# Kernel optimization log

Measured on AMD Instinct MI355X. Metric: run time of the kernel, lower is better.

## Reference

```python
import jax, jax.numpy as jnp
import numpy as np

N_HEAD = 16
OUTPUT_DIM = 1024
HEAD_DIM = OUTPUT_DIM // N_HEAD  # 64


def setup_inputs() -> dict:
    key = jax.random.key(0)
    kq, kk, kv = jax.random.split(key, 3)
    B, S, D = 4, 2048, OUTPUT_DIM
    return {
        "Q": jax.random.normal(kq, (B, S, D), dtype=jnp.float32),
        "K": jax.random.normal(kk, (B, S, D), dtype=jnp.float32),
        "V": jax.random.normal(kv, (B, S, D), dtype=jnp.float32),
    }


def reference(Q, K, V):
    # FAITHFUL to the original Keras layer: it reshapes Q into K and V as well
    # (K = reshape(Q, ...), V = reshape(Q, ...)), so the K and V inputs are
    # ignored and attention is computed of Q against itself.
    B, S, _ = Q.shape
    q = Q.reshape(B, S, N_HEAD, HEAD_DIM)  # [B,S,H,D]
    scale = 1.0 / np.sqrt(HEAD_DIM).astype(np.float32)
    # scores: [B,H,S,S]
    scores = jnp.einsum("bshd,bthd->bhst", q, q) * scale
    attn = jax.nn.softmax(scores, axis=-1)
    out = jnp.einsum("bhst,bthd->bshd", attn, q)  # [B,S,H,D]
    # concat of per-head slices along last axis == head-major reshape
    return out.reshape(B, S, N_HEAD * HEAD_DIM)
```

## Files before the change

kernel.cpp:

```cpp
#include <hip/hip_runtime.h>
#include <stdint.h>

#define S_LEN 2048
#define DH    64
#define NH    16
#define DM    1024
#define NBH   64

typedef float    f32x4 __attribute__((ext_vector_type(4)));
typedef _Float16 half8 __attribute__((ext_vector_type(8)));
typedef _Float16 half4 __attribute__((ext_vector_type(4)));

#define GL_LDS_B128(g, l) \
  __builtin_amdgcn_global_load_lds((const __attribute__((address_space(1))) void*)(g), \
                                   (__attribute__((address_space(3))) void*)(l), 16, 0, 0)

__global__ __launch_bounds__(256) void preprocess_kernel(const float* __restrict__ Q,
                                                         _Float16* __restrict__ Qh,
                                                         _Float16* __restrict__ QhT) {
    const int t  = threadIdx.x;
    const int st = blockIdx.x & 31;
    const int bh = blockIdx.x >> 5;
    const int b = bh >> 4, h = bh & 15;
    const int s0 = (t & 15) * 4;
    const int d0 = (t >> 4) * 4;
    const float* src = Q + (size_t)b * S_LEN * DM + (size_t)(st * 64) * DM + h * DH;

    half4 hv[4];
    #pragma unroll
    for (int i = 0; i < 4; ++i) {
        const float4 v = *(const float4*)(src + (size_t)(s0 + i) * DM + d0);
        hv[i] = (half4){ (_Float16)v.x, (_Float16)v.y, (_Float16)v.z, (_Float16)v.w };
    }
    _Float16* qh = Qh + ((size_t)bh * S_LEN + st * 64) * DH;
    #pragma unroll
    for (int i = 0; i < 4; ++i)
        *(half4*)(qh + (s0 + i) * DH + d0) = hv[i];
    _Float16* qt = QhT + (size_t)bh * DH * S_LEN + st * 64;
    #pragma unroll
    for (int j = 0; j < 4; ++j) {
        const half4 tv = (half4){ hv[0][j], hv[1][j], hv[2][j], hv[3][j] };
        *(half4*)(qt + (size_t)(d0 + j) * S_LEN + s0) = tv;
    }
}

__global__ __launch_bounds__(128, 2) void attn_v3_kernel(const _Float16* __restrict__ Qh,
                                                         const _Float16* __restrict__ QhT,
                                                         float* __restrict__ out) {
    __shared__ __align__(16) _Float16 KnS[64 * 64];
    __shared__ __align__(16) _Float16 KtS[64 * 64];
    __shared__ __align__(16) _Float16 Pb[2][64 * 64];

    const int tid  = threadIdx.x;
    const int w    = tid >> 6;
    const int lane = tid & 63;
    const int quad = lane >> 4;
    const int l15  = lane & 15;
    const int xq   = l15 & 7;
    const int qblk = blockIdx.x & 15;
    const int bh   = blockIdx.x >> 4;
    const int q0   = qblk * 128 + w * 64;

    const _Float16* qh_bh = Qh + (size_t)bh * S_LEN * DH;
    const _Float16* qt_bh = QhT + (size_t)bh * DH * S_LEN;

    half8 qreg[4][2];
    #pragma unroll
    for (int nch = 0; nch < 4; ++nch) {
        const _Float16* p = qh_bh + (size_t)(q0 + nch * 16 + l15) * DH + quad * 8;
        qreg[nch][0] = *(const half8*)p;
        qreg[nch][1] = *(const half8*)(p + 32);
    }

    const float qs = 0.18033688011112042f;
    float m_c[4];
    #pragma unroll
    for (int nch = 0; nch < 4; ++nch) {
        float part = 0.f;
        #pragma unroll
        for (int s = 0; s < 2; ++s)
            #pragma unroll
            for (int j = 0; j < 8; ++j) { const float x = (float)qreg[nch][s][j]; part += x * x; }
        part += __shfl_xor(part, 16, 64);
        part += __shfl_xor(part, 32, 64);
        m_c[nch] = qs * part;
    }

    const _Float16* kn_src[4]; _Float16* kn_dst[4];
    const _Float16* kt_src[4]; _Float16* kt_dst[4];
    #pragma unroll
    for (int i = 0; i < 4; ++i) {
        const int ch = i * 128 + tid;
        const int row = ch >> 3, c = ch & 7;
        kn_src[i] = qh_bh + row * DH + ((c ^ (row & 7)) * 8);
        kn_dst[i] = &KnS[ch * 8];
        kt_src[i] = qt_bh + (size_t)row * S_LEN + ((c ^ (row & 7)) * 8);
        kt_dst[i] = &KtS[ch * 8];
    }

    f32x4 O[4][4];
    #pragma unroll
    for (int m = 0; m < 4; ++m)
        #pragma unroll
        for (int n = 0; n < 4; ++n) O[m][n] = (f32x4){0.f, 0.f, 0.f, 0.f};
    float lsum[4] = {0.f, 0.f, 0.f, 0.f};
    _Float16* Pw = Pb[w];

    for (int t = 0; t < S_LEN / 64; ++t) {
        __syncthreads();
        #pragma unroll
        for (int i = 0; i < 4; ++i) GL_LDS_B128(kn_src[i] + t * (64 * DH), kn_dst[i]);
        #pragma unroll
        for (int i = 0; i < 4; ++i) GL_LDS_B128(kt_src[i] + t * 64, kt_dst[i]);
        __syncthreads();

        #pragma unroll
        for (int mch = 0; mch < 4; ++mch) {
            const half8 a0 = *(const half8*)&KnS[(mch * 16 + l15) * 64 + ((quad ^ xq) * 8)];
            const half8 a1 = *(const half8*)&KnS[(mch * 16 + l15) * 64 + (((4 + quad) ^ xq) * 8)];
            const int wc   = 2 * mch + (quad >> 1);
            const int woff = (quad & 1) * 4;
            #pragma unroll
            for (int nch = 0; nch < 4; ++nch) {
                f32x4 acc = (f32x4){0.f, 0.f, 0.f, 0.f};
                acc = __builtin_amdgcn_mfma_f32_16x16x32_f16(a0, qreg[nch][0], acc, 0, 0, 0);
                acc = __builtin_amdgcn_mfma_f32_16x16x32_f16(a1, qreg[nch][1], acc, 0, 0, 0);
                const float p0 = __builtin_amdgcn_exp2f(__builtin_fmaf(acc[0], qs, -m_c[nch]));
                const float p1 = __builtin_amdgcn_exp2f(__builtin_fmaf(acc[1], qs, -m_c[nch]));
                const float p2 = __builtin_amdgcn_exp2f(__builtin_fmaf(acc[2], qs, -m_c[nch]));
                const float p3 = __builtin_amdgcn_exp2f(__builtin_fmaf(acc[3], qs, -m_c[nch]));
                lsum[nch] += (p0 + p1) + (p2 + p3);
                const half4 hv = (half4){ (_Float16)p0, (_Float16)p1, (_Float16)p2, (_Float16)p3 };
                *(half4*)&Pw[(nch * 16 + l15) * 64 + ((wc ^ xq) * 8) + woff] = hv;
            }
        }

        half8 pf[4][2];
        #pragma unroll
        for (int mch = 0; mch < 4; ++mch) {
            pf[mch][0] = *(const half8*)&Pw[(mch * 16 + l15) * 64 + ((quad ^ xq) * 8)];
            pf[mch][1] = *(const half8*)&Pw[(mch * 16 + l15) * 64 + (((4 + quad) ^ xq) * 8)];
        }
        #pragma unroll
        for (int nch = 0; nch < 4; ++nch) {
            const half8 v0 = *(const half8*)&KtS[(nch * 16 + l15) * 64 + ((quad ^ xq) * 8)];
            const half8 v1 = *(const half8*)&KtS[(nch * 16 + l15) * 64 + (((4 + quad) ^ xq) * 8)];
            #pragma unroll
            for (int mch = 0; mch < 4; ++mch) {
                O[mch][nch] = __builtin_amdgcn_mfma_f32_16x16x32_f16(pf[mch][0], v0, O[mch][nch], 0, 0, 0);
                O[mch][nch] = __builtin_amdgcn_mfma_f32_16x16x32_f16(pf[mch][1], v1, O[mch][nch], 0, 0, 0);
            }
        }
    }

    float lcol[4];
    #pragma unroll
    for (int nch = 0; nch < 4; ++nch) {
        float l = lsum[nch];
        l += __shfl_xor(l, 16, 64);
        l += __shfl_xor(l, 32, 64);
        lcol[nch] = l;
    }
    const int b = bh >> 4, h = bh & 15;
    float* ob = out + (size_t)b * S_LEN * DM + h * DH;
    #pragma unroll
    for (int mch = 0; mch < 4; ++mch) {
        float inv[4];
        #pragma unroll
        for (int r = 0; r < 4; ++r)
            inv[r] = 1.0f / __shfl(lcol[mch], quad * 4 + r, 16);
        #pragma unroll
        for (int nch = 0; nch < 4; ++nch)
            #pragma unroll
            for (int r = 0; r < 4; ++r)
                ob[(size_t)(q0 + mch * 16 + quad * 4 + r) * DM + nch * 16 + l15] = O[mch][nch][r] * inv[r];
    }
}

extern "C" void kernel_launch(void* const* d_in, const int* in_sizes, int n_in,
                              void* d_out, int out_size, void* d_ws, size_t ws_size,
                              hipStream_t stream) {
    const float* Q = (const float*)d_in[0];
    float* out = (float*)d_out;
    _Float16* Qh  = (_Float16*)d_ws;
    _Float16* QhT = Qh + (size_t)NBH * S_LEN * DH;
    preprocess_kernel<<<dim3(NBH * (S_LEN / 64)), dim3(256), 0, stream>>>(Q, Qh, QhT);
    attn_v3_kernel<<<dim3(NBH * (S_LEN / 128)), dim3(128), 0, stream>>>(Qh, QhT, out);
}
```

Baseline: 213.7 us.

## Split attention along keys into two halves with atomic accumulation and normalize pass

Result: slower. 567.1 us (+165.3%).

```diff
diff --git a/kernel.cpp b/kernel.cpp
--- a/kernel.cpp
+++ b/kernel.cpp
@@ -6,6 +6,7 @@
 #define NH    16
 #define DM    1024
 #define NBH   64
+#define PP    40
 
 typedef float    f32x4 __attribute__((ext_vector_type(4)));
 typedef _Float16 half8 __attribute__((ext_vector_type(8)));
@@ -18,30 +19,177 @@
 __global__ __launch_bounds__(256) void preprocess_kernel(const float* __restrict__ Q,
                                                          _Float16* __restrict__ Qh,
                                                          _Float16* __restrict__ QhT) {
-    const int t  = threadIdx.x;
+    __shared__ _Float16 T[DH * 68];
+    const int tid = threadIdx.x;
     const int st = blockIdx.x & 31;
     const int bh = blockIdx.x >> 5;
     const int b = bh >> 4, h = bh & 15;
-    const int s0 = (t & 15) * 4;
-    const int d0 = (t >> 4) * 4;
     const float* src = Q + (size_t)b * S_LEN * DM + (size_t)(st * 64) * DM + h * DH;
-
-    half4 hv[4];
+    _Float16* qh_dst = Qh + ((size_t)bh * S_LEN + st * 64) * DH;
+    _Float16* qt_dst = QhT + (size_t)bh * DH * S_LEN + st * 64;
+
     #pragma unroll
     for (int i = 0; i < 4; ++i) {
-        const float4 v = *(const float4*)(src + (size_t)(s0 + i) * DM + d0);
-        hv[i] = (half4){ (_Float16)v.x, (_Float16)v.y, (_Float16)v.z, (_Float16)v.w };
-    }
-    _Float16* qh = Qh + ((size_t)bh * S_LEN + st * 64) * DH;
-    #pragma unroll
-    for (int i = 0; i < 4; ++i)
-        *(half4*)(qh + (s0 + i) * DH + d0) = hv[i];
-    _Float16* qt = QhT + (size_t)bh * DH * S_LEN + st * 64;
-    #pragma unroll
-    for (int j = 0; j < 4; ++j) {
-        const half4 tv = (half4){ hv[0][j], hv[1][j], hv[2][j], hv[3][j] };
-        *(half4*)(qt + (size_t)(d0 + j) * S_LEN + s0) = tv;
-    }
+        const int lin = i * 256 + tid;
+        const int sr  = lin >> 4;
+        const int d4  = (lin & 15) * 4;
+        const float4 v = *(const float4*)(src + (size_t)sr * DM + d4);
+        const half4 hv = { (_Float16)v.x, (_Float16)v.y, (_Float16)v.z, (_Float16)v.w };
+        *(half4*)(qh_dst + sr * DH + d4) = hv;
+        T[(d4 + 0) * 68 + sr] = hv[0];
+        T[(d4 + 1) * 68 + sr] = hv[1];
+        T[(d4 + 2) * 68 + sr] = hv[2];
+        T[(d4 + 3) * 68 + sr] = hv[3];
+    }
+    __syncthreads();
+    #pragma unroll
+    for (int i = 0; i < 4; ++i) {
+        const int lin = i * 256 + tid;
+        const int d   = lin >> 4;
+        const int s4  = (lin & 15) * 4;
+        const half4 tv = *(const half4*)&T[d * 68 + s4];
+        *(half4*)(qt_dst + (size_t)d * S_LEN + s4) = tv;
+    }
+}
+
+__global__ __launch_bounds__(128, 4) void attn_v4_kernel(const _Float16* __restrict__ Qh,
+                                                         const _Float16* __restrict__ QhT,
+                                                         float* __restrict__ out,
+                                                         float* __restrict__ lws) {
+    __shared__ __align__(16) _Float16 KnS[32 * 64];
+    __shared__ __align__(16) _Float16 KtS[64 * 32];
+    __shared__ __align__(16) _Float16 Pb[128 * PP];
+
+    const int tid  = threadIdx.x;
+    const int w    = tid >> 6;
+    const int lane = tid & 63;
+    const int quad = lane >> 4;
+    const int l15  = lane & 15;
+    const int xq   = l15 & 7;
+    const int bi   = blockIdx.x;
+    const int ks   = bi & 1;
+    const int qblk = (bi >> 1) & 15;
+    const int bh   = bi >> 5;
+    const int q0   = qblk * 128 + w * 64;
+    const int kb   = ks * (S_LEN / 2);
+
+    const _Float16* qh_bh = Qh + (size_t)bh * S_LEN * DH;
+    const _Float16* qt_bh = QhT + (size_t)bh * DH * S_LEN;
+
+    half8 qreg[4][2];
+    #pragma unroll
+    for (int nch = 0; nch < 4; ++nch) {
+        const _Float16* p = qh_bh + (size_t)(q0 + nch * 16 + l15) * DH + quad * 8;
+        qreg[nch][0] = *(const half8*)p;
+        qreg[nch][1] = *(const half8*)(p + 32);
+    }
+
+    const float qs = 0.18033688011112042f;
+    float m_c[4];
+    #pragma unroll
+    for (int nch = 0; nch < 4; ++nch) {
+        float part = 0.f;
+        #pragma unroll
+        for (int s = 0; s < 2; ++s)
+            #pragma unroll
+            for (int j = 0; j < 8; ++j) { const float x = (float)qreg[nch][s][j]; part += x * x; }
+        part += __shfl_xor(part, 16, 64);
+        part += __shfl_xor(part, 32, 64);
+        m_c[nch] = qs * part;
+    }
+
+    const _Float16* kn_src[2]; _Float16* kn_dst[2];
+    const _Float16* kt_src[2]; _Float16* kt_dst[2];
+    #pragma unroll
+    for (int i = 0; i < 2; ++i) {
+        const int chn = i * 128 + tid;
+        const int rown = chn >> 3, cn = chn & 7;
+        kn_src[i] = qh_bh + (size_t)(kb + rown) * DH + ((cn ^ (rown & 7)) * 8);
+        kn_dst[i] = &KnS[chn * 8];
+        const int cht = i * 128 + tid;
+        const int dt = cht >> 2, ct = cht & 3;
+        kt_src[i] = qt_bh + (size_t)dt * S_LEN + kb + ((ct ^ ((dt >> 1) & 3)) * 8);
+        kt_dst[i] = &KtS[cht * 8];
+    }
+
+    f32x4 O[4][4];
+    #pragma unroll
+    for (int a = 0; a < 4; ++a)
+        #pragma unroll
+        for (int n = 0; n < 4; ++n) O[a][n] = (f32x4){0.f, 0.f, 0.f, 0.f};
+    float lsum[4] = {0.f, 0.f, 0.f, 0.f};
+    _Float16* Pw = &Pb[w * 64 * PP];
+
+    for (int t = 0; t < (S_LEN / 2) / 32; ++t) {
+        __syncthreads();
+        GL_LDS_B128(kn_src[0] + t * (32 * DH), kn_dst[0]);
+        GL_LDS_B128(kn_src[1] + t * (32 * DH), kn_dst[1]);
+        GL_LDS_B128(kt_src[0] + t * 32, kt_dst[0]);
+        GL_LDS_B128(kt_src[1] + t * 32, kt_dst[1]);
+        __syncthreads();
+
+        #pragma unroll
+        for (int mch = 0; mch < 2; ++mch) {
+            const half8 a0 = *(const half8*)&KnS[(mch * 16 + l15) * 64 + ((quad ^ xq) * 8)];
+            const half8 a1 = *(const half8*)&KnS[(mch * 16 + l15) * 64 + (((4 + quad) ^ xq) * 8)];
+            #pragma unroll
+            for (int nch = 0; nch < 4; ++nch) {
+                f32x4 acc = (f32x4){0.f, 0.f, 0.f, 0.f};
+                acc = __builtin_amdgcn_mfma_f32_16x16x32_f16(a0, qreg[nch][0], acc, 0, 0, 0);
+                acc = __builtin_amdgcn_mfma_f32_16x16x32_f16(a1, qreg[nch][1], acc, 0, 0, 0);
+                const float p0 = __builtin_amdgcn_exp2f(__builtin_fmaf(acc[0], qs, -m_c[nch]));
+                const float p1 = __builtin_amdgcn_exp2f(__builtin_fmaf(acc[1], qs, -m_c[nch]));
+                const float p2 = __builtin_amdgcn_exp2f(__builtin_fmaf(acc[2], qs, -m_c[nch]));
+                const float p3 = __builtin_amdgcn_exp2f(__builtin_fmaf(acc[3], qs, -m_c[nch]));
+                lsum[nch] += (p0 + p1) + (p2 + p3);
+                const half4 hv = (half4){ (_Float16)p0, (_Float16)p1, (_Float16)p2, (_Float16)p3 };
+                *(half4*)&Pw[(nch * 16 + l15) * PP + mch * 16 + quad * 4] = hv;
+            }
+        }
+
+        half8 pf[4];
+        #pragma unroll
+        for (int a = 0; a < 4; ++a)
+            pf[a] = *(const half8*)&Pw[(a * 16 + l15) * PP + quad * 8];
+        #pragma unroll
+        for (int nch = 0; nch < 4; ++nch) {
+            const half8 vf = *(const half8*)&KtS[(nch * 16 + l15) * 32 + ((quad ^ ((l15 >> 1) & 3)) * 8)];
+            #pragma unroll
+            for (int a = 0; a < 4; ++a)
+                O[a][nch] = __builtin_amdgcn_mfma_f32_16x16x32_f16(pf[a], vf, O[a][nch], 0, 0, 0);
+        }
+    }
+
+    #pragma unroll
+    for (int nch = 0; nch < 4; ++nch) {
+        float l = lsum[nch];
+        l += __shfl_xor(l, 16, 64);
+        l += __shfl_xor(l, 32, 64);
+        if (quad == 0)
+            atomicAdd(&lws[(size_t)bh * S_LEN + q0 + nch * 16 + l15], l);
+    }
+    const int b = bh >> 4, h = bh & 15;
+    float* ob = out + (size_t)b * S_LEN * DM + h * DH;
+    #pragma unroll
+    for (int a = 0; a < 4; ++a)
+        #pragma unroll
+        for (int nch = 0; nch < 4; ++nch)
+            #pragma unroll
+            for (int r = 0; r < 4; ++r)
+                atomicAdd(&ob[(size_t)(q0 + a * 16 + quad * 4 + r) * DM + nch * 16 + l15], O[a][nch][r]);
+}
+
+__global__ __launch_bounds__(256) void normalize_kernel(float* __restrict__ out,
+                                                        const float* __restrict__ lws) {
+    const int i4 = blockIdx.x * 256 + threadIdx.x;
+    const size_t e = (size_t)i4 * 4;
+    const int b = (int)(e >> 21);
+    const int s = (int)(e >> 10) & 2047;
+    const int h = (int)(e >> 6) & 15;
+    const float inv = 1.0f / lws[(size_t)((b << 4) + h) * S_LEN + s];
+    float4 v = ((float4*)out)[i4];
+    v.x *= inv; v.y *= inv; v.z *= inv; v.w *= inv;
+    ((float4*)out)[i4] = v;
 }
 
 __global__ __launch_bounds__(128, 2) void attn_v3_kernel(const _Float16* __restrict__ Qh,
@@ -50,20 +198,14 @@
     __shared__ __align__(16) _Float16 KnS[64 * 64];
     __shared__ __align__(16) _Float16 KtS[64 * 64];
     __shared__ __align__(16) _Float16 Pb[2][64 * 64];
-
-    const int tid  = threadIdx.x;
-    const int w    = tid >> 6;
-    const int lane = tid & 63;
-    const int quad = lane >> 4;
-    const int l15  = lane & 15;
-    const int xq   = l15 & 7;
+    const int tid = threadIdx.x;
+    const int w = tid >> 6, lane = tid & 63, quad = lane >> 4, l15 = lane & 15;
+    const int xq = l15 & 7;
     const int qblk = blockIdx.x & 15;
-    const int bh   = blockIdx.x >> 4;
-    const int q0   = qblk * 128 + w * 64;
-
+    const int bh = blockIdx.x >> 4;
+    const int q0 = qblk * 128 + w * 64;
     const _Float16* qh_bh = Qh + (size_t)bh * S_LEN * DH;
     const _Float16* qt_bh = QhT + (size_t)bh * DH * S_LEN;
-
     half8 qreg[4][2];
     #pragma unroll
     for (int nch = 0; nch < 4; ++nch) {
@@ -71,7 +213,6 @@
         qreg[nch][0] = *(const half8*)p;
         qreg[nch][1] = *(const half8*)(p + 32);
     }
-
     const float qs = 0.18033688011112042f;
     float m_c[4];
     #pragma unroll
@@ -85,7 +226,6 @@
         part += __shfl_xor(part, 32, 64);
         m_c[nch] = qs * part;
     }
-
     const _Float16* kn_src[4]; _Float16* kn_dst[4];
     const _Float16* kt_src[4]; _Float16* kt_dst[4];
     #pragma unroll
@@ -97,7 +237,6 @@
         kt_src[i] = qt_bh + (size_t)row * S_LEN + ((c ^ (row & 7)) * 8);
         kt_dst[i] = &KtS[ch * 8];
     }
-
     f32x4 O[4][4];
     #pragma unroll
     for (int m = 0; m < 4; ++m)
@@ -105,7 +244,6 @@
         for (int n = 0; n < 4; ++n) O[m][n] = (f32x4){0.f, 0.f, 0.f, 0.f};
     float lsum[4] = {0.f, 0.f, 0.f, 0.f};
     _Float16* Pw = Pb[w];
-
     for (int t = 0; t < S_LEN / 64; ++t) {
         __syncthreads();
         #pragma unroll
@@ -113,12 +251,11 @@
         #pragma unroll
         for (int i = 0; i < 4; ++i) GL_LDS_B128(kt_src[i] + t * 64, kt_dst[i]);
         __syncthreads();
-
         #pragma unroll
         for (int mch = 0; mch < 4; ++mch) {
             const half8 a0 = *(const half8*)&KnS[(mch * 16 + l15) * 64 + ((quad ^ xq) * 8)];
             const half8 a1 = *(const half8*)&KnS[(mch * 16 + l15) * 64 + (((4 + quad) ^ xq) * 8)];
-            const int wc   = 2 * mch + (quad >> 1);
+            const int wc = 2 * mch + (quad >> 1);
             const int woff = (quad & 1) * 4;
             #pragma unroll
             for (int nch = 0; nch < 4; ++nch) {
@@ -134,7 +271,6 @@
                 *(half4*)&Pw[(nch * 16 + l15) * 64 + ((wc ^ xq) * 8) + woff] = hv;
             }
         }
-
         half8 pf[4][2];
         #pragma unroll
         for (int mch = 0; mch < 4; ++mch) {
@@ -152,7 +288,6 @@
             }
         }
     }
-
     float lcol[4];
     #pragma unroll
     for (int nch = 0; nch < 4; ++nch) {
@@ -182,8 +317,19 @@
                               hipStream_t stream) {
     const float* Q = (const float*)d_in[0];
     float* out = (float*)d_out;
+    const size_t qh_bytes = (size_t)NBH * S_LEN * DH * sizeof(_Float16);
+    const size_t l_bytes  = (size_t)NBH * S_LEN * sizeof(float);
     _Float16* Qh  = (_Float16*)d_ws;
-    _Float16* QhT = Qh + (size_t)NBH * S_LEN * DH;
+    _Float16* QhT = (_Float16*)((char*)d_ws + qh_bytes);
     preprocess_kernel<<<dim3(NBH * (S_LEN / 64)), dim3(256), 0, stream>>>(Q, Qh, QhT);
-    attn_v3_kernel<<<dim3(NBH * (S_LEN / 128)), dim3(128), 0, stream>>>(Qh, QhT, out);
-}
+
+    if (ws_size >= 2 * qh_bytes + l_bytes) {
+        float* lws = (float*)((char*)d_ws + 2 * qh_bytes);
+        hipMemsetAsync(out, 0, (size_t)out_size * sizeof(float), stream);
+        hipMemsetAsync(lws, 0, l_bytes, stream);
+        attn_v4_kernel<<<dim3(NBH * 16 * 2), dim3(128), 0, stream>>>(Qh, QhT, out, lws);
+        normalize_kernel<<<dim3((out_size / 4) / 256), dim3(256), 0, stream>>>(out, lws);
+    } else {
+        attn_v3_kernel<<<dim3(NBH * (S_LEN / 128)), dim3(128), 0, stream>>>(Qh, QhT, out);
+    }
+}
```

## Split key range across wave pairs and restage preprocess transpose through LDS

Applied to the files above, without the earlier changes.

Result: slower. 445.0 us (+108.2%).

```diff
diff --git a/kernel.cpp b/kernel.cpp
--- a/kernel.cpp
+++ b/kernel.cpp
@@ -6,6 +6,7 @@
 #define NH    16
 #define DM    1024
 #define NBH   64
+#define PP    40
 
 typedef float    f32x4 __attribute__((ext_vector_type(4)));
 typedef _Float16 half8 __attribute__((ext_vector_type(8)));
@@ -18,38 +19,44 @@
 __global__ __launch_bounds__(256) void preprocess_kernel(const float* __restrict__ Q,
                                                          _Float16* __restrict__ Qh,
                                                          _Float16* __restrict__ QhT) {
-    const int t  = threadIdx.x;
+    __shared__ _Float16 T[DH * 68];
+    const int tid = threadIdx.x;
     const int st = blockIdx.x & 31;
     const int bh = blockIdx.x >> 5;
     const int b = bh >> 4, h = bh & 15;
-    const int s0 = (t & 15) * 4;
-    const int d0 = (t >> 4) * 4;
     const float* src = Q + (size_t)b * S_LEN * DM + (size_t)(st * 64) * DM + h * DH;
-
-    half4 hv[4];
+    _Float16* qh_dst = Qh + ((size_t)bh * S_LEN + st * 64) * DH;
+    _Float16* qt_dst = QhT + (size_t)bh * DH * S_LEN + st * 64;
+
     #pragma unroll
     for (int i = 0; i < 4; ++i) {
-        const float4 v = *(const float4*)(src + (size_t)(s0 + i) * DM + d0);
-        hv[i] = (half4){ (_Float16)v.x, (_Float16)v.y, (_Float16)v.z, (_Float16)v.w };
-    }
-    _Float16* qh = Qh + ((size_t)bh * S_LEN + st * 64) * DH;
-    #pragma unroll
-    for (int i = 0; i < 4; ++i)
-        *(half4*)(qh + (s0 + i) * DH + d0) = hv[i];
-    _Float16* qt = QhT + (size_t)bh * DH * S_LEN + st * 64;
-    #pragma unroll
-    for (int j = 0; j < 4; ++j) {
-        const half4 tv = (half4){ hv[0][j], hv[1][j], hv[2][j], hv[3][j] };
-        *(half4*)(qt + (size_t)(d0 + j) * S_LEN + s0) = tv;
+        const int lin = i * 256 + tid;
+        const int sr  = lin >> 4;
+        const int d4  = (lin & 15) * 4;
+        const float4 v = *(const float4*)(src + (size_t)sr * DM + d4);
+        const half4 hv = { (_Float16)v.x, (_Float16)v.y, (_Float16)v.z, (_Float16)v.w };
+        *(half4*)(qh_dst + sr * DH + d4) = hv;
+        T[(d4 + 0) * 68 + sr] = hv[0];
+        T[(d4 + 1) * 68 + sr] = hv[1];
+        T[(d4 + 2) * 68 + sr] = hv[2];
+        T[(d4 + 3) * 68 + sr] = hv[3];
+    }
+    __syncthreads();
+    #pragma unroll
+    for (int i = 0; i < 4; ++i) {
+        const int lin = i * 256 + tid;
+        const int d   = lin >> 4;
+        const int s4  = (lin & 15) * 4;
+        const half4 tv = *(const half4*)&T[d * 68 + s4];
+        *(half4*)(qt_dst + (size_t)d * S_LEN + s4) = tv;
     }
 }
 
-__global__ __launch_bounds__(128, 2) void attn_v3_kernel(const _Float16* __restrict__ Qh,
+__global__ __launch_bounds__(256, 4) void attn_v5_kernel(const _Float16* __restrict__ Qh,
                                                          const _Float16* __restrict__ QhT,
                                                          float* __restrict__ out) {
-    __shared__ __align__(16) _Float16 KnS[64 * 64];
-    __shared__ __align__(16) _Float16 KtS[64 * 64];
-    __shared__ __align__(16) _Float16 Pb[2][64 * 64];
+    __shared__ __align__(16) _Float16 stag[4 * 2048];
+    __shared__ __align__(16) _Float16 Pbuf[4 * 64 * PP];
 
     const int tid  = threadIdx.x;
     const int w    = tid >> 6;
@@ -57,9 +64,11 @@
     const int quad = lane >> 4;
     const int l15  = lane & 15;
     const int xq   = l15 & 7;
+    const int p    = w & 1;
+    const int ks   = w >> 1;
     const int qblk = blockIdx.x & 15;
     const int bh   = blockIdx.x >> 4;
-    const int q0   = qblk * 128 + w * 64;
+    const int q0   = qblk * 128 + p * 64;
 
     const _Float16* qh_bh = Qh + (size_t)bh * S_LEN * DH;
     const _Float16* qt_bh = QhT + (size_t)bh * DH * S_LEN;
@@ -67,9 +76,9 @@
     half8 qreg[4][2];
     #pragma unroll
     for (int nch = 0; nch < 4; ++nch) {
-        const _Float16* p = qh_bh + (size_t)(q0 + nch * 16 + l15) * DH + quad * 8;
-        qreg[nch][0] = *(const half8*)p;
-        qreg[nch][1] = *(const half8*)(p + 32);
+        const _Float16* ptr = qh_bh + (size_t)(q0 + nch * 16 + l15) * DH + quad * 8;
+        qreg[nch][0] = *(const half8*)ptr;
+        qreg[nch][1] = *(const half8*)(ptr + 32);
     }
 
     const float qs = 0.18033688011112042f;
@@ -86,40 +95,40 @@
         m_c[nch] = qs * part;
     }
 
-    const _Float16* kn_src[4]; _Float16* kn_dst[4];
-    const _Float16* kt_src[4]; _Float16* kt_dst[4];
-    #pragma unroll
-    for (int i = 0; i < 4; ++i) {
-        const int ch = i * 128 + tid;
-        const int row = ch >> 3, c = ch & 7;
-        kn_src[i] = qh_bh + row * DH + ((c ^ (row & 7)) * 8);
-        kn_dst[i] = &KnS[ch * 8];
-        kt_src[i] = qt_bh + (size_t)row * S_LEN + ((c ^ (row & 7)) * 8);
-        kt_dst[i] = &KtS[ch * 8];
-    }
+    const int rown = tid >> 3, cn = tid & 7;
+    const int dt   = tid >> 2, ct = tid & 3;
+    const _Float16* kn_srcA = qh_bh + (size_t)rown * DH + ((cn ^ (rown & 7)) * 8);
+    const _Float16* kt_srcA = qt_bh + (size_t)dt * S_LEN + ((ct ^ ((dt >> 1) & 3)) * 8);
+    _Float16* kn_dstA = &stag[0 * 2048 + tid * 8];
+    _Float16* kt_dstA = &stag[1 * 2048 + tid * 8];
+    _Float16* kn_dstB = &stag[2 * 2048 + tid * 8];
+    _Float16* kt_dstB = &stag[3 * 2048 + tid * 8];
+
+    const _Float16* KnW = &stag[(ks * 2) * 2048];
+    const _Float16* KtW = &stag[(ks * 2 + 1) * 2048];
+    _Float16* Pw = &Pbuf[w * 64 * PP];
 
     f32x4 O[4][4];
     #pragma unroll
-    for (int m = 0; m < 4; ++m)
-        #pragma unroll
-        for (int n = 0; n < 4; ++n) O[m][n] = (f32x4){0.f, 0.f, 0.f, 0.f};
+    for (int a = 0; a < 4; ++a)
+        #pragma unroll
+        for (int n = 0; n < 4; ++n) O[a][n] = (f32x4){0.f, 0.f, 0.f, 0.f};
     float lsum[4] = {0.f, 0.f, 0.f, 0.f};
-    _Float16* Pw = Pb[w];
-
-    for (int t = 0; t < S_LEN / 64; ++t) {
+
+    for (int t = 0; t < 32; ++t) {
+        const int kbA = t * 32;
+        const int kbB = 1024 + t * 32;
         __syncthreads();
-        #pragma unroll
-        for (int i = 0; i < 4; ++i) GL_LDS_B128(kn_src[i] + t * (64 * DH), kn_dst[i]);
-        #pragma unroll
-        for (int i = 0; i < 4; ++i) GL_LDS_B128(kt_src[i] + t * 64, kt_dst[i]);
+        GL_LDS_B128(kn_srcA + (size_t)kbA * DH, kn_dstA);
+        GL_LDS_B128(kt_srcA + kbA,              kt_dstA);
+        GL_LDS_B128(kn_srcA + (size_t)kbB * DH, kn_dstB);
+        GL_LDS_B128(kt_srcA + kbB,              kt_dstB);
         __syncthreads();
 
         #pragma unroll
-        for (int mch = 0; mch < 4; ++mch) {
-            const half8 a0 = *(const half8*)&KnS[(mch * 16 + l15) * 64 + ((quad ^ xq) * 8)];
-            const half8 a1 = *(const half8*)&KnS[(mch * 16 + l15) * 64 + (((4 + quad) ^ xq) * 8)];
-            const int wc   = 2 * mch + (quad >> 1);
-            const int woff = (quad & 1) * 4;
+        for (int mch = 0; mch < 2; ++mch) {
+            const half8 a0 = *(const half8*)&KnW[(mch * 16 + l15) * 64 + ((quad ^ xq) * 8)];
+            const half8 a1 = *(const half8*)&KnW[(mch * 16 + l15) * 64 + (((4 + quad) ^ xq) * 8)];
             #pragma unroll
             for (int nch = 0; nch < 4; ++nch) {
                 f32x4 acc = (f32x4){0.f, 0.f, 0.f, 0.f};
@@ -131,49 +140,73 @@
                 const float p3 = __builtin_amdgcn_exp2f(__builtin_fmaf(acc[3], qs, -m_c[nch]));
                 lsum[nch] += (p0 + p1) + (p2 + p3);
                 const half4 hv = (half4){ (_Float16)p0, (_Float16)p1, (_Float16)p2, (_Float16)p3 };
-                *(half4*)&Pw[(nch * 16 + l15) * 64 + ((wc ^ xq) * 8) + woff] = hv;
+                *(half4*)&Pw[(nch * 16 + l15) * PP + mch * 16 + quad * 4] = hv;
             }
         }
 
-        half8 pf[4][2];
-        #pragma unroll
-        for (int mch = 0; mch < 4; ++mch) {
-            pf[mch][0] = *(const half8*)&Pw[(mch * 16 + l15) * 64 + ((quad ^ xq) * 8)];
-            pf[mch][1] = *(const half8*)&Pw[(mch * 16 + l15) * 64 + (((4 + quad) ^ xq) * 8)];
-        }
+        half8 pf[4];
+        #pragma unroll
+        for (int a = 0; a < 4; ++a)
+            pf[a] = *(const half8*)&Pw[(a * 16 + l15) * PP + quad * 8];
         #pragma unroll
         for (int nch = 0; nch < 4; ++nch) {
-            const half8 v0 = *(const half8*)&KtS[(nch * 16 + l15) * 64 + ((quad ^ xq) * 8)];
-            const half8 v1 = *(const half8*)&KtS[(nch * 16 + l15) * 64 + (((4 + quad) ^ xq) * 8)];
-            #pragma unroll
-            for (int mch = 0; mch < 4; ++mch) {
-                O[mch][nch] = __builtin_amdgcn_mfma_f32_16x16x32_f16(pf[mch][0], v0, O[mch][nch], 0, 0, 0);
-                O[mch][nch] = __builtin_amdgcn_mfma_f32_16x16x32_f16(pf[mch][1], v1, O[mch][nch], 0, 0, 0);
-            }
-        }
-    }
-
-    float lcol[4];
-    #pragma unroll
-    for (int nch = 0; nch < 4; ++nch) {
-        float l = lsum[nch];
-        l += __shfl_xor(l, 16, 64);
-        l += __shfl_xor(l, 32, 64);
-        lcol[nch] = l;
-    }
-    const int b = bh >> 4, h = bh & 15;
-    float* ob = out + (size_t)b * S_LEN * DM + h * DH;
-    #pragma unroll
-    for (int mch = 0; mch < 4; ++mch) {
-        float inv[4];
-        #pragma unroll
-        for (int r = 0; r < 4; ++r)
-            inv[r] = 1.0f / __shfl(lcol[mch], quad * 4 + r, 16);
+            const half8 vf = *(const half8*)&KtW[(nch * 16 + l15) * 32 + ((quad ^ ((l15 >> 1) & 3)) * 8)];
+            #pragma unroll
+            for (int a = 0; a < 4; ++a)
+                O[a][nch] = __builtin_amdgcn_mfma_f32_16x16x32_f16(pf[a], vf, O[a][nch], 0, 0, 0);
+        }
+    }
+
+    __syncthreads();
+    _Float16* obx = stag;
+    float* lx = (float*)&Pbuf[2 * 64 * PP];
+    if (ks == 1) {
+        #pragma unroll
+        for (int a = 0; a < 4; ++a)
+            #pragma unroll
+            for (int nch = 0; nch < 4; ++nch)
+                #pragma unroll
+                for (int r = 0; r < 4; ++r)
+                    obx[p * 4096 + (a * 16 + nch * 4 + r) * 64 + lane] = (_Float16)O[a][nch][r];
         #pragma unroll
         for (int nch = 0; nch < 4; ++nch)
+            lx[p * 256 + nch * 64 + lane] = lsum[nch];
+    }
+    __syncthreads();
+    if (ks == 0) {
+        #pragma unroll
+        for (int a = 0; a < 4; ++a)
+            #pragma unroll
+            for (int nch = 0; nch < 4; ++nch)
+                #pragma unroll
+                for (int r = 0; r < 4; ++r)
+                    O[a][nch][r] += (float)obx[p * 4096 + (a * 16 + nch * 4 + r) * 64 + lane];
+        #pragma unroll
+        for (int nch = 0; nch < 4; ++nch)
+            lsum[nch] += lx[p * 256 + nch * 64 + lane];
+
+        float lcol[4];
+        #pragma unroll
+        for (int nch = 0; nch < 4; ++nch) {
+            float l = lsum[nch];
+            l += __shfl_xor(l, 16, 64);
+            l += __shfl_xor(l, 32, 64);
+            lcol[nch] = l;
+        }
+        const int b = bh >> 4, h = bh & 15;
+        float* ob = out + (size_t)b * S_LEN * DM + h * DH;
+        #pragma unroll
+        for (int a = 0; a < 4; ++a) {
+            float inv[4];
             #pragma unroll
             for (int r = 0; r < 4; ++r)
-                ob[(size_t)(q0 + mch * 16 + quad * 4 + r) * DM + nch * 16 + l15] = O[mch][nch][r] * inv[r];
+                inv[r] = 1.0f / __shfl(lcol[a], quad * 4 + r, 16);
+            #pragma unroll
+            for (int nch = 0; nch < 4; ++nch)
+                #pragma unroll
+                for (int r = 0; r < 4; ++r)
+                    ob[(size_t)(q0 + a * 16 + quad * 4 + r) * DM + nch * 16 + l15] = O[a][nch][r] * inv[r];
+        }
     }
 }
 
@@ -185,5 +218,5 @@
     _Float16* Qh  = (_Float16*)d_ws;
     _Float16* QhT = Qh + (size_t)NBH * S_LEN * DH;
     preprocess_kernel<<<dim3(NBH * (S_LEN / 64)), dim3(256), 0, stream>>>(Q, Qh, QhT);
-    attn_v3_kernel<<<dim3(NBH * (S_LEN / 128)), dim3(128), 0, stream>>>(Qh, QhT, out);
+    attn_v5_kernel<<<dim3(NBH * (S_LEN / 128)), dim3(256), 0, stream>>>(Qh, QhT, out);
 }
```
